# Kernel optimization log

Hardware: AMD Instinct MI355X
Metric: run time of the kernel (lower is better)

The kernel has to match this reference:

```python
import jax, jax.numpy as jnp
import numpy as np

E = 768   # embedding_dim
D = 64    # head_dim
B = 8
S = 2048


def setup_inputs() -> dict:
    key = jax.random.key(0)
    k1, k2, k3, k4 = jax.random.split(key, 4)
    inputs = jax.random.normal(k1, (B, S, E), dtype=jnp.float32)
    # causal mask: 1 where attending allowed, 0 elsewhere (masked_fill where ==0)
    attention_mask = jnp.tril(jnp.ones((S, S), dtype=jnp.int32))[None, :, :]
    Q = jax.random.normal(k2, (E, D), dtype=jnp.float32) * 0.01
    K = jax.random.normal(k3, (E, D), dtype=jnp.float32) * 0.01
    V = jax.random.normal(k4, (E, D), dtype=jnp.float32) * 0.01
    return {"inputs": inputs, "attention_mask": attention_mask, "Q": Q, "K": K, "V": V}


def reference(inputs, attention_mask, Q, K, V):
    scale = 1.0 / np.sqrt(D).astype(np.float32)
    q = inputs @ Q          # [B,S,D]
    k = inputs @ K          # [B,S,D]
    v = inputs @ V          # [B,S,D]
    w = jnp.einsum('bqd,bkd->bqk', q, k) * scale   # [B,S,S]
    w = jnp.where(attention_mask == 0, -jnp.inf, w)
    attn = jax.nn.softmax(w, axis=-1)              # [B,S,S]
    states = attn @ v                              # [B,S,D] (dropout p=0.0 is identity)
    return states
```

## Files before the change

kernel.cpp:

```cpp
#include <hip/hip_runtime.h>
#include <cstdint>

#define B_ 8
#define S_ 2048
#define E_ 768
#define D_ 64
#define NSPLIT 4
#define SEGLEN (S_ / NSPLIT)
#define ROWS (B_ * S_)

typedef unsigned short ushort_t;
typedef __attribute__((ext_vector_type(8))) short s16x8;
typedef __attribute__((ext_vector_type(4))) float f32x4;

__device__ inline ushort_t f2bf(float f) {
  unsigned int x = __float_as_uint(f);
  return (ushort_t)((x + 0x7fffu + ((x >> 16) & 1u)) >> 16);
}

__device__ inline unsigned int pkbf(float hi, float lo) {
  return __builtin_amdgcn_perm(__float_as_uint(hi) + 0x8000u,
                               __float_as_uint(lo) + 0x8000u, 0x07060302u);
}

__device__ inline void async16(const void* g, void* l) {
  __builtin_amdgcn_global_load_lds(
      (const __attribute__((address_space(1))) unsigned int*)g,
      (__attribute__((address_space(3))) unsigned int*)l, 16, 0, 0);
}

__global__ __launch_bounds__(256) void wt_kernel(
    const float* __restrict__ Wq, const float* __restrict__ Wk,
    const float* __restrict__ Wv, ushort_t* __restrict__ wt) {
  const int mat = blockIdx.y;
  const int e = blockIdx.x * 4 + (threadIdx.x >> 6);
  const int d = threadIdx.x & 63;
  const float* W = (mat == 0) ? Wq : ((mat == 1) ? Wk : Wv);
  wt[(long)(mat * 64 + d) * E_ + e] = f2bf(W[(long)e * D_ + d]);
}

__global__ __launch_bounds__(256) void qkv_mfma(
    const float* __restrict__ in, const ushort_t* __restrict__ wt,
    ushort_t* __restrict__ qb, ushort_t* __restrict__ kb,
    ushort_t* __restrict__ vtb) {
  const int tid = threadIdx.x;
  const int w = tid >> 6;
  const int L = tid & 63;
  const int c = L & 15;
  const int q = L >> 4;
  const int row0 = blockIdx.x * 32;

  __shared__ float Alds[2][32][64];
  __shared__ ushort_t Blds[2][192][64];

  const int ar0 = w * 8 + (L >> 4);
  const int ar1 = ar0 + 4;
  const int asl = L & 15;
  const float* asrc0 = in + (long)(row0 + ar0) * E_ + ((asl ^ (ar0 & 15)) << 2);
  const float* asrc1 = in + (long)(row0 + ar1) * E_ + ((asl ^ (ar1 & 15)) << 2);
  const int bsl = L & 7;
  const ushort_t* bsrc[6];
#pragma unroll
  for (int jj = 0; jj < 6; ++jj) {
    const int br = w * 48 + jj * 8 + (L >> 3);
    bsrc[jj] = wt + (long)br * E_ + ((bsl ^ (br & 7)) << 3);
  }
  float* ad[2] = {&Alds[0][w * 8][0], &Alds[1][w * 8][0]};
  ushort_t* bd[2] = {&Blds[0][w * 48][0], &Blds[1][w * 48][0]};

  const int mloc = w & 1;
  const int nbase = (w >> 1) * 6;
  const int ra = mloc * 16 + c;
  const int offA00 = ra * 256 + ((2 * q + 0) ^ c) * 16;
  const int offA01 = ra * 256 + ((2 * q + 1) ^ c) * 16;
  const int offA10 = ra * 256 + ((8 + 2 * q + 0) ^ c) * 16;
  const int offA11 = ra * 256 + ((8 + 2 * q + 1) ^ c) * 16;
  int offB0[6], offB1[6];
#pragma unroll
  for (int t = 0; t < 6; ++t) {
    const int n = (nbase + t) * 16 + c;
    offB0[t] = n * 128 + ((q + 0) ^ (c & 7)) * 16;
    offB1[t] = n * 128 + ((q + 4) ^ (c & 7)) * 16;
  }
  const char* Abase = (const char*)&Alds[0][0][0];
  const char* Bbase = (const char*)&Blds[0][0][0];

  f32x4 acc[6];
#pragma unroll
  for (int n = 0; n < 6; ++n) acc[n] = (f32x4){0.f, 0.f, 0.f, 0.f};

  async16(asrc0, ad[0]);
  async16(asrc1, ad[0] + 4 * 64);
#pragma unroll
  for (int jj = 0; jj < 6; ++jj) async16(bsrc[jj], bd[0] + jj * 8 * 64);
  asrc0 += 64; asrc1 += 64;
#pragma unroll
  for (int jj = 0; jj < 6; ++jj) bsrc[jj] += 64;

  for (int it = 0; it < E_ / 64; ++it) {
    const int b = it & 1;
    __syncthreads();
    if (it + 1 < E_ / 64) {
      const int nb = 1 - b;
      async16(asrc0, ad[nb]);
      async16(asrc1, ad[nb] + 4 * 64);
#pragma unroll
      for (int jj = 0; jj < 6; ++jj) async16(bsrc[jj], bd[nb] + jj * 8 * 64);
      asrc0 += 64; asrc1 += 64;
#pragma unroll
      for (int jj = 0; jj < 6; ++jj) bsrc[jj] += 64;
    }
    const char* Ab = Abase + b * 8192;
    const char* Bb = Bbase + b * 24576;
    const float4 a00 = *(const float4*)(Ab + offA00);
    const float4 a01 = *(const float4*)(Ab + offA01);
    const float4 a10 = *(const float4*)(Ab + offA10);
    const float4 a11 = *(const float4*)(Ab + offA11);
    union { s16x8 v; unsigned int u[4]; } af0, af1;
    af0.u[0] = pkbf(a00.y, a00.x);
    af0.u[1] = pkbf(a00.w, a00.z);
    af0.u[2] = pkbf(a01.y, a01.x);
    af0.u[3] = pkbf(a01.w, a01.z);
    af1.u[0] = pkbf(a10.y, a10.x);
    af1.u[1] = pkbf(a10.w, a10.z);
    af1.u[2] = pkbf(a11.y, a11.x);
    af1.u[3] = pkbf(a11.w, a11.z);
#pragma unroll
    for (int t = 0; t < 6; ++t) {
      const s16x8 bf0 = *(const s16x8*)(Bb + offB0[t]);
      const s16x8 bf1 = *(const s16x8*)(Bb + offB1[t]);
      acc[t] = __builtin_amdgcn_mfma_f32_16x16x32_bf16(af0.v, bf0, acc[t], 0, 0, 0);
      acc[t] = __builtin_amdgcn_mfma_f32_16x16x32_bf16(af1.v, bf1, acc[t], 0, 0, 0);
    }
  }

  const float qscale = 0.125f * 1.44269504088896340736f;
  const int row0w = row0 + mloc * 16;
  const int b_ = row0w >> 11;
  const int srow = row0w & (S_ - 1);
#pragma unroll
  for (int n = 0; n < 6; ++n) {
    const int gn = nbase + n;
    const int mat = gn >> 2;
    const int d0 = (gn & 3) * 16 + c;
#pragma unroll
    for (int reg = 0; reg < 4; ++reg) {
      const int m = q * 4 + reg;
      const float x = acc[n][reg];
      if (mat == 0) {
        qb[(long)(row0w + m) * D_ + d0] = f2bf(x * qscale);
      } else if (mat == 1) {
        kb[(long)(row0w + m) * D_ + d0] = f2bf(x);
      } else {
        vtb[(long)b_ * D_ * S_ + (long)d0 * S_ + srow + m] = f2bf(x);
      }
    }
  }
}

__global__ __launch_bounds__(256) void attn_mfma(
    const ushort_t* __restrict__ qb, const ushort_t* __restrict__ kb,
    const ushort_t* __restrict__ vtb, float* __restrict__ op,
    float* __restrict__ lw) {
  const int w = threadIdx.x >> 6;
  const int L = threadIdx.x & 63;
  const int col = L & 15;
  const int quad = L >> 4;

  const int task = blockIdx.x * 4 + w;
  const int batch = task / 320;
  const int r = task % 320;
  int seg, qtl;
  if (r < 128)      { seg = 0; qtl = r; }
  else if (r < 224) { seg = 1; qtl = r - 96; }
  else if (r < 288) { seg = 2; qtl = r - 160; }
  else              { seg = 3; qtl = r - 192; }

  const int j0 = seg * SEGLEN;
  const int q0 = qtl * 16;
  const int jmax = min(j0 + SEGLEN, q0 + 16);
  const int ntiles = (jmax - j0 + 63) >> 6;

  __shared__ ushort_t Pl[4][16][72];

  const ushort_t* kbb = kb + (long)batch * S_ * D_;
  const ushort_t* vbb = vtb + (long)batch * D_ * S_;
  const ushort_t* qrow = qb + (long)(batch * S_ + q0 + col) * D_;
  const s16x8 qf0 = *(const s16x8*)(qrow + quad * 8);
  const s16x8 qf1 = *(const s16x8*)(qrow + 32 + quad * 8);

  f32x4 O[4];
#pragma unroll
  for (int t = 0; t < 4; ++t) O[t] = (f32x4){0.f, 0.f, 0.f, 0.f};
  float l[4] = {0.f, 0.f, 0.f, 0.f};

  for (int i = 0; i < ntiles; ++i) {
    const int kt = j0 + i * 64;
    s16x8 kf0[4], kf1[4], vf0[4], vf1[4];
#pragma unroll
    for (int t = 0; t < 4; ++t) {
      const ushort_t* kr = kbb + ((long)(kt + t * 16 + col) << 6) + quad * 8;
      kf0[t] = *(const s16x8*)kr;
      kf1[t] = *(const s16x8*)(kr + 32);
    }
#pragma unroll
    for (int t = 0; t < 4; ++t) {
      const ushort_t* vr = vbb + (long)(t * 16 + col) * S_ + kt + quad * 8;
      vf0[t] = *(const s16x8*)vr;
      vf1[t] = *(const s16x8*)(vr + 32);
    }
    f32x4 Sv[4];
#pragma unroll
    for (int t = 0; t < 4; ++t) {
      f32x4 z = (f32x4){0.f, 0.f, 0.f, 0.f};
      z = __builtin_amdgcn_mfma_f32_16x16x32_bf16(qf0, kf0[t], z, 0, 0, 0);
      Sv[t] = __builtin_amdgcn_mfma_f32_16x16x32_bf16(qf1, kf1[t], z, 0, 0, 0);
    }
    if (kt + 63 > q0) {
#pragma unroll
      for (int t = 0; t < 4; ++t) {
        const int colg = kt + t * 16 + col;
#pragma unroll
        for (int reg = 0; reg < 4; ++reg) {
          const int rowg = q0 + quad * 4 + reg;
          if (colg > rowg) Sv[t][reg] = -1e30f;
        }
      }
    }
    float P[4][4];
#pragma unroll
    for (int t = 0; t < 4; ++t)
#pragma unroll
      for (int reg = 0; reg < 4; ++reg) {
        P[t][reg] = exp2f(Sv[t][reg]);
        l[reg] += P[t][reg];
      }
#pragma unroll
    for (int t = 0; t < 4; ++t)
#pragma unroll
      for (int reg = 0; reg < 4; ++reg)
        Pl[w][quad * 4 + reg][t * 16 + col] = f2bf(P[t][reg]);
    const s16x8 p0 = *(const s16x8*)&Pl[w][col][quad * 8];
    const s16x8 p1 = *(const s16x8*)&Pl[w][col][32 + quad * 8];
#pragma unroll
    for (int t = 0; t < 4; ++t) {
      O[t] = __builtin_amdgcn_mfma_f32_16x16x32_bf16(p0, vf0[t], O[t], 0, 0, 0);
      O[t] = __builtin_amdgcn_mfma_f32_16x16x32_bf16(p1, vf1[t], O[t], 0, 0, 0);
    }
  }
#pragma unroll
  for (int off = 1; off < 16; off <<= 1)
#pragma unroll
    for (int reg = 0; reg < 4; ++reg)
      l[reg] += __shfl_xor(l[reg], off);

  const int growbase = batch * S_ + q0;
#pragma unroll
  for (int t = 0; t < 4; ++t)
#pragma unroll
    for (int reg = 0; reg < 4; ++reg)
      op[((long)seg * ROWS + growbase + quad * 4 + reg) * D_ + t * 16 + col] =
          O[t][reg];
  if (col == 0) {
#pragma unroll
    for (int reg = 0; reg < 4; ++reg)
      lw[(long)seg * ROWS + growbase + quad * 4 + reg] = l[reg];
  }
}

__global__ __launch_bounds__(256) void attn_combine(
    const float* __restrict__ op, const float* __restrict__ lw,
    float* __restrict__ out) {
  const int t = threadIdx.x;
  const int d = t & 63;
  const int g = blockIdx.x * 4 + (t >> 6);
  const int s_q = g & (S_ - 1);
  float osum = 0.f, lsum = 0.f;
#pragma unroll
  for (int s = 0; s < NSPLIT; ++s) {
    if (s_q >= s * SEGLEN) {
      osum += op[((long)s * ROWS + g) * D_ + d];
      lsum += lw[(long)s * ROWS + g];
    }
  }
  out[(long)g * D_ + d] = osum / lsum;
}

extern "C" void kernel_launch(void* const* d_in, const int* in_sizes, int n_in,
                              void* d_out, int out_size, void* d_ws, size_t ws_size,
                              hipStream_t stream) {
  const float* in = (const float*)d_in[0];
  const float* Wq = (const float*)d_in[2];
  const float* Wk = (const float*)d_in[3];
  const float* Wv = (const float*)d_in[4];
  float* out = (float*)d_out;

  ushort_t* qbuf = (ushort_t*)d_ws;
  ushort_t* kbuf = qbuf + (long)ROWS * D_;
  ushort_t* vtb = kbuf + (long)ROWS * D_;
  float* op = (float*)(vtb + (long)ROWS * D_);
  float* lw = op + (long)NSPLIT * ROWS * D_;
  ushort_t* wt = (ushort_t*)(lw + (long)NSPLIT * ROWS);

  wt_kernel<<<dim3(E_ / 4, 3), 256, 0, stream>>>(Wq, Wk, Wv, wt);
  qkv_mfma<<<ROWS / 32, 256, 0, stream>>>(in, wt, qbuf, kbuf, vtb);
  attn_mfma<<<640, 256, 0, stream>>>(qbuf, kbuf, vtb, op, lw);
  attn_combine<<<(ROWS * D_) / 256, 256, 0, stream>>>(op, lw, out);
}
```

Measured before the change: 162.8 us.

## Double-buffer K/V register loads in attention and enlarge QKV projection tiles

The attention loop now prefetches the next K/V tile into a second register set while the current tile is computed, wraps the MFMA sections in raised wave priority, and asks for two blocks per CU through launch bounds. This is meant to hide global-load latency behind the tensor-core work. The QKV projection moves from 32-row, 256-thread blocks to 64-row, 512-thread blocks, so each block reuses the shared weight tile across twice as many rows. The costs are higher register pressure in attention, which the two-blocks-per-CU bound may turn into spills, and fewer but larger projection blocks.

```diff
diff --git a/kernel.cpp b/kernel.cpp
--- a/kernel.cpp
+++ b/kernel.cpp
@@ -39,7 +39,7 @@
   wt[(long)(mat * 64 + d) * E_ + e] = f2bf(W[(long)e * D_ + d]);
 }
 
-__global__ __launch_bounds__(256) void qkv_mfma(
+__global__ __launch_bounds__(512) void qkv_mfma(
     const float* __restrict__ in, const ushort_t* __restrict__ wt,
     ushort_t* __restrict__ qb, ushort_t* __restrict__ kb,
     ushort_t* __restrict__ vtb) {
@@ -48,9 +48,9 @@
   const int L = tid & 63;
   const int c = L & 15;
   const int q = L >> 4;
-  const int row0 = blockIdx.x * 32;
-
-  __shared__ float Alds[2][32][64];
+  const int row0 = blockIdx.x * 64;
+
+  __shared__ float Alds[2][64][64];
   __shared__ ushort_t Blds[2][192][64];
 
   const int ar0 = w * 8 + (L >> 4);
@@ -59,17 +59,17 @@
   const float* asrc0 = in + (long)(row0 + ar0) * E_ + ((asl ^ (ar0 & 15)) << 2);
   const float* asrc1 = in + (long)(row0 + ar1) * E_ + ((asl ^ (ar1 & 15)) << 2);
   const int bsl = L & 7;
-  const ushort_t* bsrc[6];
-#pragma unroll
-  for (int jj = 0; jj < 6; ++jj) {
-    const int br = w * 48 + jj * 8 + (L >> 3);
+  const ushort_t* bsrc[3];
+#pragma unroll
+  for (int jj = 0; jj < 3; ++jj) {
+    const int br = w * 24 + jj * 8 + (L >> 3);
     bsrc[jj] = wt + (long)br * E_ + ((bsl ^ (br & 7)) << 3);
   }
   float* ad[2] = {&Alds[0][w * 8][0], &Alds[1][w * 8][0]};
-  ushort_t* bd[2] = {&Blds[0][w * 48][0], &Blds[1][w * 48][0]};
-
-  const int mloc = w & 1;
-  const int nbase = (w >> 1) * 6;
+  ushort_t* bd[2] = {&Blds[0][w * 24][0], &Blds[1][w * 24][0]};
+
+  const int mloc = w & 3;
+  const int nbase = (w >> 2) * 6;
   const int ra = mloc * 16 + c;
   const int offA00 = ra * 256 + ((2 * q + 0) ^ c) * 16;
   const int offA01 = ra * 256 + ((2 * q + 1) ^ c) * 16;
@@ -92,10 +92,10 @@
   async16(asrc0, ad[0]);
   async16(asrc1, ad[0] + 4 * 64);
 #pragma unroll
-  for (int jj = 0; jj < 6; ++jj) async16(bsrc[jj], bd[0] + jj * 8 * 64);
+  for (int jj = 0; jj < 3; ++jj) async16(bsrc[jj], bd[0] + jj * 8 * 64);
   asrc0 += 64; asrc1 += 64;
 #pragma unroll
-  for (int jj = 0; jj < 6; ++jj) bsrc[jj] += 64;
+  for (int jj = 0; jj < 3; ++jj) bsrc[jj] += 64;
 
   for (int it = 0; it < E_ / 64; ++it) {
     const int b = it & 1;
@@ -105,12 +105,12 @@
       async16(asrc0, ad[nb]);
       async16(asrc1, ad[nb] + 4 * 64);
 #pragma unroll
-      for (int jj = 0; jj < 6; ++jj) async16(bsrc[jj], bd[nb] + jj * 8 * 64);
+      for (int jj = 0; jj < 3; ++jj) async16(bsrc[jj], bd[nb] + jj * 8 * 64);
       asrc0 += 64; asrc1 += 64;
 #pragma unroll
-      for (int jj = 0; jj < 6; ++jj) bsrc[jj] += 64;
-    }
-    const char* Ab = Abase + b * 8192;
+      for (int jj = 0; jj < 3; ++jj) bsrc[jj] += 64;
+    }
+    const char* Ab = Abase + b * 16384;
     const char* Bb = Bbase + b * 24576;
     const float4 a00 = *(const float4*)(Ab + offA00);
     const float4 a01 = *(const float4*)(Ab + offA01);
@@ -158,7 +158,60 @@
   }
 }
 
-__global__ __launch_bounds__(256) void attn_mfma(
+#define LOADKV(K0, K1, V0, V1, KT)                                            \
+  {                                                                           \
+    for (int t = 0; t < 4; ++t) {                                             \
+      const ushort_t* kr =                                                    \
+          kbb + ((long)((KT) + t * 16 + col) << 6) + quad * 8;                \
+      K0[t] = *(const s16x8*)kr;                                              \
+      K1[t] = *(const s16x8*)(kr + 32);                                       \
+      const ushort_t* vr =                                                    \
+          vbb + (long)(t * 16 + col) * S_ + (KT) + quad * 8;                  \
+      V0[t] = *(const s16x8*)vr;                                              \
+      V1[t] = *(const s16x8*)(vr + 32);                                       \
+    }                                                                         \
+    __builtin_amdgcn_sched_barrier(0);     \
+  }
+
+#define TILE(K0, K1, V0, V1, KT)                                              \
+  {                                                                           \
+    f32x4 Sv[4];                                                              \
+    __builtin_amdgcn_s_setprio(1);                                            \
+    for (int t = 0; t < 4; ++t) {                                             \
+      f32x4 z = (f32x4){0.f, 0.f, 0.f, 0.f};                                  \
+      z = __builtin_amdgcn_mfma_f32_16x16x32_bf16(qf0, K0[t], z, 0, 0, 0);    \
+      Sv[t] = __builtin_amdgcn_mfma_f32_16x16x32_bf16(qf1, K1[t], z, 0, 0, 0);\
+    }                                                                         \
+    __builtin_amdgcn_s_setprio(0);                                            \
+    if ((KT) + 63 > q0) {                                                     \
+      for (int t = 0; t < 4; ++t) {                                           \
+        const int colg = (KT) + t * 16 + col;                                 \
+        for (int reg = 0; reg < 4; ++reg) {                                   \
+          const int rowg = q0 + quad * 4 + reg;                               \
+          if (colg > rowg) Sv[t][reg] = -1e30f;                               \
+        }                                                                     \
+      }                                                                       \
+    }                                                                         \
+    float Pv[4][4];                                                           \
+    for (int t = 0; t < 4; ++t)                                               \
+      for (int reg = 0; reg < 4; ++reg) {                                     \
+        Pv[t][reg] = exp2f(Sv[t][reg]);                                       \
+        l[reg] += Pv[t][reg];                                                 \
+      }                                                                       \
+    for (int t = 0; t < 4; ++t)                                               \
+      for (int reg = 0; reg < 4; ++reg)                                       \
+        Pl[w][quad * 4 + reg][t * 16 + col] = f2bf(Pv[t][reg]);               \
+    const s16x8 p0 = *(const s16x8*)&Pl[w][col][quad * 8];                    \
+    const s16x8 p1 = *(const s16x8*)&Pl[w][col][32 + quad * 8];               \
+    __builtin_amdgcn_s_setprio(1);                                            \
+    for (int t = 0; t < 4; ++t) {                                             \
+      O[t] = __builtin_amdgcn_mfma_f32_16x16x32_bf16(p0, V0[t], O[t], 0, 0, 0);\
+      O[t] = __builtin_amdgcn_mfma_f32_16x16x32_bf16(p1, V1[t], O[t], 0, 0, 0);\
+    }                                                                         \
+    __builtin_amdgcn_s_setprio(0);                                            \
+  }
+
+__global__ __launch_bounds__(256, 2) void attn_mfma(
     const ushort_t* __restrict__ qb, const ushort_t* __restrict__ kb,
     const ushort_t* __restrict__ vtb, float* __restrict__ op,
     float* __restrict__ lw) {
@@ -175,7 +228,6 @@
   else if (r < 224) { seg = 1; qtl = r - 96; }
   else if (r < 288) { seg = 2; qtl = r - 160; }
   else              { seg = 3; qtl = r - 192; }
-
   const int j0 = seg * SEGLEN;
   const int q0 = qtl * 16;
   const int jmax = min(j0 + SEGLEN, q0 + 16);
@@ -194,60 +246,26 @@
   for (int t = 0; t < 4; ++t) O[t] = (f32x4){0.f, 0.f, 0.f, 0.f};
   float l[4] = {0.f, 0.f, 0.f, 0.f};
 
-  for (int i = 0; i < ntiles; ++i) {
-    const int kt = j0 + i * 64;
-    s16x8 kf0[4], kf1[4], vf0[4], vf1[4];
-#pragma unroll
-    for (int t = 0; t < 4; ++t) {
-      const ushort_t* kr = kbb + ((long)(kt + t * 16 + col) << 6) + quad * 8;
-      kf0[t] = *(const s16x8*)kr;
-      kf1[t] = *(const s16x8*)(kr + 32);
-    }
-#pragma unroll
-    for (int t = 0; t < 4; ++t) {
-      const ushort_t* vr = vbb + (long)(t * 16 + col) * S_ + kt + quad * 8;
-      vf0[t] = *(const s16x8*)vr;
-      vf1[t] = *(const s16x8*)(vr + 32);
-    }
-    f32x4 Sv[4];
-#pragma unroll
-    for (int t = 0; t < 4; ++t) {
-      f32x4 z = (f32x4){0.f, 0.f, 0.f, 0.f};
-      z = __builtin_amdgcn_mfma_f32_16x16x32_bf16(qf0, kf0[t], z, 0, 0, 0);
-      Sv[t] = __builtin_amdgcn_mfma_f32_16x16x32_bf16(qf1, kf1[t], z, 0, 0, 0);
-    }
-    if (kt + 63 > q0) {
-#pragma unroll
-      for (int t = 0; t < 4; ++t) {
-        const int colg = kt + t * 16 + col;
-#pragma unroll
-        for (int reg = 0; reg < 4; ++reg) {
-          const int rowg = q0 + quad * 4 + reg;
-          if (colg > rowg) Sv[t][reg] = -1e30f;
-        }
-      }
-    }
-    float P[4][4];
-#pragma unroll
-    for (int t = 0; t < 4; ++t)
-#pragma unroll
-      for (int reg = 0; reg < 4; ++reg) {
-        P[t][reg] = exp2f(Sv[t][reg]);
-        l[reg] += P[t][reg];
-      }
-#pragma unroll
-    for (int t = 0; t < 4; ++t)
-#pragma unroll
-      for (int reg = 0; reg < 4; ++reg)
-        Pl[w][quad * 4 + reg][t * 16 + col] = f2bf(P[t][reg]);
-    const s16x8 p0 = *(const s16x8*)&Pl[w][col][quad * 8];
-    const s16x8 p1 = *(const s16x8*)&Pl[w][col][32 + quad * 8];
-#pragma unroll
-    for (int t = 0; t < 4; ++t) {
-      O[t] = __builtin_amdgcn_mfma_f32_16x16x32_bf16(p0, vf0[t], O[t], 0, 0, 0);
-      O[t] = __builtin_amdgcn_mfma_f32_16x16x32_bf16(p1, vf1[t], O[t], 0, 0, 0);
-    }
-  }
+  s16x8 kA0[4], kA1[4], vA0[4], vA1[4];
+  s16x8 kB0[4], kB1[4], vB0[4], vB1[4];
+
+  LOADKV(kA0, kA1, vA0, vA1, j0);
+  int i = 0;
+  for (;;) {
+    {
+      const int kt = j0 + i * 64;
+      if (i + 1 < ntiles) LOADKV(kB0, kB1, vB0, vB1, kt + 64);
+      TILE(kA0, kA1, vA0, vA1, kt);
+      if (++i >= ntiles) break;
+    }
+    {
+      const int kt = j0 + i * 64;
+      if (i + 1 < ntiles) LOADKV(kA0, kA1, vA0, vA1, kt + 64);
+      TILE(kB0, kB1, vB0, vB1, kt);
+      if (++i >= ntiles) break;
+    }
+  }
+
 #pragma unroll
   for (int off = 1; off < 16; off <<= 1)
 #pragma unroll
@@ -303,7 +321,7 @@
   ushort_t* wt = (ushort_t*)(lw + (long)NSPLIT * ROWS);
 
   wt_kernel<<<dim3(E_ / 4, 3), 256, 0, stream>>>(Wq, Wk, Wv, wt);
-  qkv_mfma<<<ROWS / 32, 256, 0, stream>>>(in, wt, qbuf, kbuf, vtb);
+  qkv_mfma<<<ROWS / 64, 512, 0, stream>>>(in, wt, qbuf, kbuf, vtb);
   attn_mfma<<<640, 256, 0, stream>>>(qbuf, kbuf, vtb, op, lw);
   attn_combine<<<(ROWS * D_) / 256, 256, 0, stream>>>(op, lw, out);
 }
```

After: 161.8 us. Within noise of the previous version (-0.6%).
